# Performance work log

Measured on AMD Instinct MI355X. Metric: run time of the kernel, lower is better.

## Reference

```python
import jax, jax.numpy as jnp
import numpy as np

N_NODES = 50000


def _gcn_conv(x, W, b, src, dst, n):
    # GCNConv (PyG semantics): x' = D^-1/2 (A + I) D^-1/2 (x W) + b
    h = x @ W  # [N, out]
    loop = jnp.arange(n, dtype=src.dtype)
    s = jnp.concatenate([src, loop])  # self-loops appended
    d = jnp.concatenate([dst, loop])
    deg = jax.ops.segment_sum(jnp.ones_like(d, dtype=h.dtype), d, num_segments=n)
    dinv = jnp.where(deg > 0, jax.lax.rsqrt(deg), 0.0)
    norm = dinv[s] * dinv[d]  # [E+N]
    msgs = norm[:, None] * h[s]  # gather: [E+N, out]
    out = jax.ops.segment_sum(msgs, d, num_segments=n)  # scatter-add
    return out + b


def setup_inputs() -> dict:
    key = jax.random.key(0)
    ks = jax.random.split(key, 6)
    n, din, dh, dout, e = N_NODES, 64, 64, 16, 1600000
    x = jax.random.normal(ks[0], (n, din), dtype=jnp.float32)
    edge_index = jax.random.randint(ks[1], (2, e), 0, n, dtype=jnp.int64)
    W1 = jax.random.normal(ks[2], (din, dh), dtype=jnp.float32) / np.sqrt(din)
    b1 = jnp.zeros((dh,), dtype=jnp.float32)
    W2 = jax.random.normal(ks[3], (dh, dout), dtype=jnp.float32) / np.sqrt(dh)
    b2 = jnp.zeros((dout,), dtype=jnp.float32)
    return {"x": x, "edge_index": edge_index, "W1": W1, "b1": b1, "W2": W2, "b2": b2}


def reference(x, edge_index, W1, b1, W2, b2):
    n = x.shape[0]
    src, dst = edge_index[0], edge_index[1]
    h = _gcn_conv(x, W1, b1, src, dst, n)
    h = jax.nn.relu(h)
    h = _gcn_conv(h, W2, b2, src, dst, n)
    return jax.nn.log_softmax(h, axis=1)
```

## Files before the change

### kernel.cpp

```cpp
#include <hip/hip_runtime.h>
#include <hip/hip_bf16.h>
#include <math.h>

#define BSHIFT 6
#define BNODES 64
#define MAXB 1024
#define SORTCAP 4096

__device__ __forceinline__ bool detect_f64(const void* edges, long long nn) {
    const long long* e64 = (const long long*)edges;
    bool ok = true;
#pragma unroll
    for (int i = 0; i < 8; ++i) {
        long long v = e64[i];
        ok = ok && (v >= 0 && v < nn);
    }
    return ok;
}

__device__ __forceinline__ float bf16lo(unsigned int u) {
    return __uint_as_float(u << 16);
}
__device__ __forceinline__ float bf16hi(unsigned int u) {
    return __uint_as_float(u & 0xFFFF0000u);
}
__device__ __forceinline__ float bf16dec(unsigned short u) {
    return __uint_as_float(((unsigned int)u) << 16);
}
__device__ __forceinline__ unsigned short bf16enc(float f) {
    __hip_bfloat16 h = __float2bfloat16(f);
    return *reinterpret_cast<unsigned short*>(&h);
}

__global__ __launch_bounds__(512) void k_hist(const void* edges, long long nn,
                                              long long E, long long epb,
                                              int nbuckets, int nblk, int* partial) {
    __shared__ int cnt[MAXB];
    int t = threadIdx.x;
    int i = blockIdx.x;
    for (int b = t; b < nbuckets; b += 512) cnt[b] = 0;
    __syncthreads();
    bool f64 = detect_f64(edges, nn);
    long long e0 = (long long)i * epb;
    long long e1 = e0 + epb; if (e1 > E) e1 = E;
    for (long long e = e0 + t; e < e1; e += 512) {
        int d = f64 ? (int)((const long long*)edges)[E + e] : ((const int*)edges)[E + e];
        atomicAdd(&cnt[d >> BSHIFT], 1);
    }
    __syncthreads();
    for (int b = t; b < nbuckets; b += 512) partial[b * nblk + i] = cnt[b];
}

__global__ __launch_bounds__(512) void k_scanB(int* partial, int nblk, int* totals) {
    __shared__ int tmp[512];
    int b = blockIdx.x, t = threadIdx.x;
    int v = (t < nblk) ? partial[b * nblk + t] : 0;
    tmp[t] = v;
    __syncthreads();
    for (int off = 1; off < 512; off <<= 1) {
        int a = (t >= off) ? tmp[t - off] : 0;
        __syncthreads();
        tmp[t] += a;
        __syncthreads();
    }
    if (t < nblk) partial[b * nblk + t] = tmp[t] - v;
    if (t == 511) totals[b] = tmp[511];
}

__global__ __launch_bounds__(1024) void k_scan(const int* __restrict__ totals, int nbuckets,
                                               int* base) {
    __shared__ int tmp[MAXB];
    int t = threadIdx.x;
    int v = (t < nbuckets) ? totals[t] : 0;
    tmp[t] = v;
    __syncthreads();
    for (int off = 1; off < MAXB; off <<= 1) {
        int a = (t >= off) ? tmp[t - off] : 0;
        __syncthreads();
        tmp[t] += a;
        __syncthreads();
    }
    if (t < nbuckets) base[t] = tmp[t] - v;
}

__global__ __launch_bounds__(512) void k_place(const void* edges, long long nn,
                                               long long E, long long epb,
                                               int nbuckets, int nblk,
                                               const int* __restrict__ base,
                                               const int* __restrict__ partial,
                                               unsigned int* keys) {
    __shared__ int cur[MAXB];
    int t = threadIdx.x;
    int i = blockIdx.x;
    for (int b = t; b < nbuckets; b += 512) cur[b] = base[b] + partial[b * nblk + i];
    __syncthreads();
    bool f64 = detect_f64(edges, nn);
    long long e0 = (long long)i * epb;
    long long e1 = e0 + epb; if (e1 > E) e1 = E;
    for (long long e = e0 + t; e < e1; e += 512) {
        int s, d;
        if (f64) {
            const long long* ee = (const long long*)edges;
            s = (int)ee[e]; d = (int)ee[E + e];
        } else {
            const int* ee = (const int*)edges;
            s = ee[e]; d = ee[E + e];
        }
        int pos = atomicAdd(&cur[d >> BSHIFT], 1);
        keys[pos] = (unsigned int)s | ((unsigned int)(d & (BNODES - 1)) << 17);
    }
}

__global__ __launch_bounds__(256) void k_sortdeg(unsigned int* keys,
                                                 const int* __restrict__ base,
                                                 const int* __restrict__ totals,
                                                 int* rowstart, int* counts,
                                                 float* dinv, int n,
                                                 unsigned int* scratch) {
    __shared__ unsigned int kbuf[SORTCAP];
    __shared__ int hist[BNODES];
    __shared__ int cur[BNODES];
    int t = threadIdx.x;
    int bk = blockIdx.x;
    int st = base[bk], c = totals[bk];
    if (t < BNODES) hist[t] = 0;
    __syncthreads();
    bool fits = (c <= SORTCAP);
    if (fits) {
        for (int i = t; i < c; i += 256) {
            unsigned int k = keys[st + i];
            kbuf[i] = k;
            atomicAdd(&hist[k >> 17], 1);
        }
    } else {
        for (int i = t; i < c; i += 256) {
            unsigned int k = keys[st + i];
            scratch[st + i] = k;
            atomicAdd(&hist[k >> 17], 1);
        }
    }
    __syncthreads();
    if (t < 64) {
        int v = hist[t];
        int incl = v;
        for (int o = 1; o < 64; o <<= 1) {
            int other = __shfl_up(incl, o, 64);
            if (t >= o) incl += other;
        }
        int ex = incl - v;
        cur[t] = ex;
        int node = bk * BNODES + t;
        if (node < n) {
            rowstart[node] = st + ex;
            counts[node] = v;
            dinv[node] = rsqrtf((float)v + 1.0f);
        }
    }
    __syncthreads();
    if (fits) {
        for (int i = t; i < c; i += 256) {
            unsigned int k = kbuf[i];
            int pos = atomicAdd(&cur[k >> 17], 1);
            keys[st + pos] = k & 0x1FFFFu;
        }
    } else {
        for (int i = t; i < c; i += 256) {
            unsigned int k = scratch[st + i];
            int pos = atomicAdd(&cur[k >> 17], 1);
            keys[st + pos] = k & 0x1FFFFu;
        }
    }
}

__global__ __launch_bounds__(256) void k_gemm1(const float* __restrict__ x,
                                               const float* __restrict__ W,
                                               const float* __restrict__ dinv,
                                               unsigned short* __restrict__ h) {
    __shared__ float Ws[64][64];
    __shared__ float xs[16][64];
    int t = threadIdx.x;
    for (int i = t; i < 64 * 64; i += 256) Ws[i >> 6][i & 63] = W[i];
    long long row0 = (long long)blockIdx.x * 16;
    ((float4*)xs)[t] = ((const float4*)(x + row0 * 64))[t];
    __syncthreads();
    int r = t >> 4, c0 = (t & 15) * 4;
    float4 acc = {0.f, 0.f, 0.f, 0.f};
#pragma unroll
    for (int k = 0; k < 64; ++k) {
        float xv = xs[r][k];
        float4 wv = *((const float4*)&Ws[k][c0]);
        acc.x += xv * wv.x; acc.y += xv * wv.y;
        acc.z += xv * wv.z; acc.w += xv * wv.w;
    }
    float di = dinv[row0 + r];
    ushort4 pk;
    pk.x = bf16enc(di * acc.x);
    pk.y = bf16enc(di * acc.y);
    pk.z = bf16enc(di * acc.z);
    pk.w = bf16enc(di * acc.w);
    *((ushort4*)(h + (row0 + r) * 64 + c0)) = pk;
}

__global__ __launch_bounds__(256) void k_agg64(const int* __restrict__ rowstart,
                                               const int* __restrict__ counts,
                                               const unsigned int* __restrict__ srcs,
                                               const uint2* __restrict__ hb4,
                                               const float* __restrict__ dinv,
                                               const float* __restrict__ b,
                                               const float* __restrict__ W2,
                                               unsigned short* __restrict__ h2b, int n) {
    __shared__ float W2s[64 * 17];
    int t = threadIdx.x;
    for (int i = t; i < 64 * 16; i += 256) W2s[(i >> 4) * 17 + (i & 15)] = W2[i];
    __syncthreads();

    int d = (blockIdx.x * 256 + t) >> 6;
    if (d >= n) return;
    int lane = t & 63;
    unsigned int q = lane >> 4;
    unsigned int fl = lane & 15;
    float a0 = 0.f, a1 = 0.f, a2 = 0.f, a3 = 0.f;
    if (q == 0) {
        uint2 u = hb4[(unsigned int)d * 16u + fl];
        a0 = bf16lo(u.x); a1 = bf16hi(u.x); a2 = bf16lo(u.y); a3 = bf16hi(u.y);
    }
    int start = rowstart[d];
    int cnt = counts[d];
    int k = 0;
    for (; k + 16 <= cnt; k += 16) {
        unsigned int s0 = srcs[start + k + q];
        unsigned int s1 = srcs[start + k + 4 + q];
        unsigned int s2 = srcs[start + k + 8 + q];
        unsigned int s3 = srcs[start + k + 12 + q];
        uint2 u0 = hb4[s0 * 16u + fl];
        uint2 u1 = hb4[s1 * 16u + fl];
        uint2 u2 = hb4[s2 * 16u + fl];
        uint2 u3 = hb4[s3 * 16u + fl];
        a0 += bf16lo(u0.x); a1 += bf16hi(u0.x); a2 += bf16lo(u0.y); a3 += bf16hi(u0.y);
        a0 += bf16lo(u1.x); a1 += bf16hi(u1.x); a2 += bf16lo(u1.y); a3 += bf16hi(u1.y);
        a0 += bf16lo(u2.x); a1 += bf16hi(u2.x); a2 += bf16lo(u2.y); a3 += bf16hi(u2.y);
        a0 += bf16lo(u3.x); a1 += bf16hi(u3.x); a2 += bf16lo(u3.y); a3 += bf16hi(u3.y);
    }
    for (; k + 8 <= cnt; k += 8) {
        unsigned int s0 = srcs[start + k + q];
        unsigned int s1 = srcs[start + k + 4 + q];
        uint2 u0 = hb4[s0 * 16u + fl];
        uint2 u1 = hb4[s1 * 16u + fl];
        a0 += bf16lo(u0.x); a1 += bf16hi(u0.x); a2 += bf16lo(u0.y); a3 += bf16hi(u0.y);
        a0 += bf16lo(u1.x); a1 += bf16hi(u1.x); a2 += bf16lo(u1.y); a3 += bf16hi(u1.y);
    }
    for (; k < cnt; k += 4) {
        int idx = k + (int)q;
        if (idx < cnt) {
            uint2 u0 = hb4[srcs[start + idx] * 16u + fl];
            a0 += bf16lo(u0.x); a1 += bf16hi(u0.x); a2 += bf16lo(u0.y); a3 += bf16hi(u0.y);
        }
    }
    a0 += __shfl_xor(a0, 16); a0 += __shfl_xor(a0, 32);
    a1 += __shfl_xor(a1, 16); a1 += __shfl_xor(a1, 32);
    a2 += __shfl_xor(a2, 16); a2 += __shfl_xor(a2, 32);
    a3 += __shfl_xor(a3, 16); a3 += __shfl_xor(a3, 32);
    float di = dinv[d];
    float4 bb = ((const float4*)b)[fl];
    float o0 = fmaxf(di * a0 + bb.x, 0.f);
    float o1 = fmaxf(di * a1 + bb.y, 0.f);
    float o2 = fmaxf(di * a2 + bb.z, 0.f);
    float o3 = fmaxf(di * a3 + bb.w, 0.f);

    int c = lane & 15;
    float acc = 0.f;
#pragma unroll
    for (int j = 0; j < 16; ++j) {
        int kk = (int)q * 16 + j;
        int srcl = (int)q * 20 + (j >> 2);
        float fv;
        if ((j & 3) == 0)      fv = __shfl(o0, srcl);
        else if ((j & 3) == 1) fv = __shfl(o1, srcl);
        else if ((j & 3) == 2) fv = __shfl(o2, srcl);
        else                   fv = __shfl(o3, srcl);
        acc += fv * W2s[kk * 17 + c];
    }
    acc += __shfl_xor(acc, 16);
    acc += __shfl_xor(acc, 32);
    if (lane < 16) h2b[(unsigned int)d * 16u + c] = bf16enc(di * acc);
}

__global__ __launch_bounds__(256) void k_agg16(const int* __restrict__ rowstart,
                                               const int* __restrict__ counts,
                                               const unsigned int* __restrict__ srcs,
                                               const uint2* __restrict__ hb4,
                                               const float* __restrict__ dinv,
                                               const float* __restrict__ b,
                                               float* __restrict__ out, int n) {
    int g = (blockIdx.x * 256 + threadIdx.x) >> 4;
    if (g >= n) return;
    int lane = threadIdx.x & 15;
    unsigned int eg = lane >> 2;
    unsigned int fp = lane & 3;
    float a0 = 0.f, a1 = 0.f, a2 = 0.f, a3 = 0.f;
    if (eg == 0) {
        uint2 u = hb4[(unsigned int)g * 4u + fp];
        a0 = bf16lo(u.x); a1 = bf16hi(u.x); a2 = bf16lo(u.y); a3 = bf16hi(u.y);
    }
    int start = rowstart[g];
    int cnt = counts[g];
    int k = 0;
    for (; k + 8 <= cnt; k += 8) {
        unsigned int s0 = srcs[start + k + eg];
        unsigned int s1 = srcs[start + k + 4 + eg];
        uint2 u0 = hb4[s0 * 4u + fp];
        uint2 u1 = hb4[s1 * 4u + fp];
        a0 += bf16lo(u0.x); a1 += bf16hi(u0.x); a2 += bf16lo(u0.y); a3 += bf16hi(u0.y);
        a0 += bf16lo(u1.x); a1 += bf16hi(u1.x); a2 += bf16lo(u1.y); a3 += bf16hi(u1.y);
    }
    for (; k < cnt; k += 4) {
        int idx = k + (int)eg;
        if (idx < cnt) {
            uint2 u0 = hb4[srcs[start + idx] * 4u + fp];
            a0 += bf16lo(u0.x); a1 += bf16hi(u0.x); a2 += bf16lo(u0.y); a3 += bf16hi(u0.y);
        }
    }
    a0 += __shfl_xor(a0, 4); a0 += __shfl_xor(a0, 8);
    a1 += __shfl_xor(a1, 4); a1 += __shfl_xor(a1, 8);
    a2 += __shfl_xor(a2, 4); a2 += __shfl_xor(a2, 8);
    a3 += __shfl_xor(a3, 4); a3 += __shfl_xor(a3, 8);
    float di = dinv[g];
    float4 bb = ((const float4*)b)[fp];
    float v0 = di * a0 + bb.x;
    float v1 = di * a1 + bb.y;
    float v2 = di * a2 + bb.z;
    float v3 = di * a3 + bb.w;
    float m = fmaxf(fmaxf(v0, v1), fmaxf(v2, v3));
    m = fmaxf(m, __shfl_xor(m, 1));
    m = fmaxf(m, __shfl_xor(m, 2));
    float ex = __expf(v0 - m) + __expf(v1 - m) + __expf(v2 - m) + __expf(v3 - m);
    ex += __shfl_xor(ex, 1);
    ex += __shfl_xor(ex, 2);
    float lse = __logf(ex) + m;
    if (eg == 0) {
        float4 o4;
        o4.x = v0 - lse; o4.y = v1 - lse; o4.z = v2 - lse; o4.w = v3 - lse;
        ((float4*)(out + (unsigned int)g * 16u))[fp] = o4;
    }
}

extern "C" void kernel_launch(void* const* d_in, const int* in_sizes, int n_in,
                              void* d_out, int out_size, void* d_ws, size_t ws_size,
                              hipStream_t stream) {
    const float* x  = (const float*)d_in[0];
    const void*  ei = d_in[1];
    const float* W1 = (const float*)d_in[2];
    const float* b1 = (const float*)d_in[3];
    const float* W2 = (const float*)d_in[4];
    const float* b2 = (const float*)d_in[5];

    long long dh  = in_sizes[3];
    long long din = in_sizes[2] / dh;
    long long n   = in_sizes[0] / din;
    long long E   = (long long)in_sizes[1] / 2;
    int nbuckets  = (int)((n + BNODES - 1) >> BSHIFT);

    long long epb = 4096;
    while ((E + epb - 1) / epb > 512) epb <<= 1;
    int nblk = (int)((E + epb - 1) / epb);

    char* ws = (char*)d_ws;
    auto alloc = [&](size_t bytes) { void* p = ws; ws += (bytes + 255) & ~255ULL; return p; };
    int*   totals   = (int*)alloc(nbuckets * 4);
    int*   base     = (int*)alloc(nbuckets * 4);
    int*   rowstart = (int*)alloc(n * 4);
    int*   counts   = (int*)alloc(n * 4);
    float* dinv     = (float*)alloc(n * 4);
    int*   partial  = (int*)alloc((size_t)nbuckets * nblk * 4);
    unsigned int* keys = (unsigned int*)alloc(E * 4);
    unsigned short* h1b  = (unsigned short*)alloc(n * 64 * 2);
    unsigned short* h2b  = (unsigned short*)alloc(n * 16 * 2);
    unsigned int* sort_scratch = (unsigned int*)h1b;

    float* out = (float*)d_out;

    k_hist<<<nblk, 512, 0, stream>>>(ei, n, E, epb, nbuckets, nblk, partial);
    k_scanB<<<nbuckets, 512, 0, stream>>>(partial, nblk, totals);
    k_scan<<<1, 1024, 0, stream>>>(totals, nbuckets, base);
    k_place<<<nblk, 512, 0, stream>>>(ei, n, E, epb, nbuckets, nblk, base, partial, keys);
    k_sortdeg<<<nbuckets, 256, 0, stream>>>(keys, base, totals, rowstart, counts,
                                            dinv, (int)n, sort_scratch);

    k_gemm1<<<(int)(n / 16), 256, 0, stream>>>(x, W1, dinv, h1b);
    k_agg64<<<(int)((n * 64 + 255) / 256), 256, 0, stream>>>(
        rowstart, counts, keys, (const uint2*)h1b, dinv, b1, W2, h2b, (int)n);

    k_agg16<<<(int)((n * 16 + 255) / 256), 256, 0, stream>>>(
        rowstart, counts, keys, (const uint2*)h2b, dinv, b2, out, (int)n);
}
```

Baseline: 119.3 us.

## Halve histogram blocks, deepen agg64 unroll, and restructure agg16 per-feature lanes

Edge blocks per histogram/place pass drop from at most 512 to at most 256, with the per-bucket scan shrunk to 256 threads to match. k_agg64 gains a 32-edge unrolled loop to keep more gathers in flight. k_agg16 now gives each lane one feature across all edges instead of splitting edges across lane groups. That removes the cross-lane reduction but issues scalar 2-byte gathers and redundant index loads. Fewer histogram blocks reduce scan work but may lower parallelism in hist/place.

```diff
diff --git a/kernel.cpp b/kernel.cpp
--- a/kernel.cpp
+++ b/kernel.cpp
@@ -51,20 +51,20 @@
     for (int b = t; b < nbuckets; b += 512) partial[b * nblk + i] = cnt[b];
 }
 
-__global__ __launch_bounds__(512) void k_scanB(int* partial, int nblk, int* totals) {
-    __shared__ int tmp[512];
+__global__ __launch_bounds__(256) void k_scanB(int* partial, int nblk, int* totals) {
+    __shared__ int tmp[256];
     int b = blockIdx.x, t = threadIdx.x;
     int v = (t < nblk) ? partial[b * nblk + t] : 0;
     tmp[t] = v;
     __syncthreads();
-    for (int off = 1; off < 512; off <<= 1) {
+    for (int off = 1; off < 256; off <<= 1) {
         int a = (t >= off) ? tmp[t - off] : 0;
         __syncthreads();
         tmp[t] += a;
         __syncthreads();
     }
     if (t < nblk) partial[b * nblk + t] = tmp[t] - v;
-    if (t == 511) totals[b] = tmp[511];
+    if (t == 255) totals[b] = tmp[255];
 }
 
 __global__ __launch_bounds__(1024) void k_scan(const int* __restrict__ totals, int nbuckets,
@@ -227,6 +227,32 @@
     int start = rowstart[d];
     int cnt = counts[d];
     int k = 0;
+    for (; k + 32 <= cnt; k += 32) {
+        unsigned int s0 = srcs[start + k + q];
+        unsigned int s1 = srcs[start + k + 4 + q];
+        unsigned int s2 = srcs[start + k + 8 + q];
+        unsigned int s3 = srcs[start + k + 12 + q];
+        unsigned int s4 = srcs[start + k + 16 + q];
+        unsigned int s5 = srcs[start + k + 20 + q];
+        unsigned int s6 = srcs[start + k + 24 + q];
+        unsigned int s7 = srcs[start + k + 28 + q];
+        uint2 u0 = hb4[s0 * 16u + fl];
+        uint2 u1 = hb4[s1 * 16u + fl];
+        uint2 u2 = hb4[s2 * 16u + fl];
+        uint2 u3 = hb4[s3 * 16u + fl];
+        uint2 u4 = hb4[s4 * 16u + fl];
+        uint2 u5 = hb4[s5 * 16u + fl];
+        uint2 u6 = hb4[s6 * 16u + fl];
+        uint2 u7 = hb4[s7 * 16u + fl];
+        a0 += bf16lo(u0.x); a1 += bf16hi(u0.x); a2 += bf16lo(u0.y); a3 += bf16hi(u0.y);
+        a0 += bf16lo(u1.x); a1 += bf16hi(u1.x); a2 += bf16lo(u1.y); a3 += bf16hi(u1.y);
+        a0 += bf16lo(u2.x); a1 += bf16hi(u2.x); a2 += bf16lo(u2.y); a3 += bf16hi(u2.y);
+        a0 += bf16lo(u3.x); a1 += bf16hi(u3.x); a2 += bf16lo(u3.y); a3 += bf16hi(u3.y);
+        a0 += bf16lo(u4.x); a1 += bf16hi(u4.x); a2 += bf16lo(u4.y); a3 += bf16hi(u4.y);
+        a0 += bf16lo(u5.x); a1 += bf16hi(u5.x); a2 += bf16lo(u5.y); a3 += bf16hi(u5.y);
+        a0 += bf16lo(u6.x); a1 += bf16hi(u6.x); a2 += bf16lo(u6.y); a3 += bf16hi(u6.y);
+        a0 += bf16lo(u7.x); a1 += bf16hi(u7.x); a2 += bf16lo(u7.y); a3 += bf16hi(u7.y);
+    }
     for (; k + 16 <= cnt; k += 16) {
         unsigned int s0 = srcs[start + k + q];
         unsigned int s1 = srcs[start + k + 4 + q];
@@ -288,60 +314,46 @@
 __global__ __launch_bounds__(256) void k_agg16(const int* __restrict__ rowstart,
                                                const int* __restrict__ counts,
                                                const unsigned int* __restrict__ srcs,
-                                               const uint2* __restrict__ hb4,
+                                               const unsigned short* __restrict__ hb,
                                                const float* __restrict__ dinv,
                                                const float* __restrict__ b,
                                                float* __restrict__ out, int n) {
     int g = (blockIdx.x * 256 + threadIdx.x) >> 4;
     if (g >= n) return;
-    int lane = threadIdx.x & 15;
-    unsigned int eg = lane >> 2;
-    unsigned int fp = lane & 3;
-    float a0 = 0.f, a1 = 0.f, a2 = 0.f, a3 = 0.f;
-    if (eg == 0) {
-        uint2 u = hb4[(unsigned int)g * 4u + fp];
-        a0 = bf16lo(u.x); a1 = bf16hi(u.x); a2 = bf16lo(u.y); a3 = bf16hi(u.y);
-    }
+    unsigned int f = threadIdx.x & 15;
+    float acc = bf16dec(hb[(unsigned int)g * 16u + f]);
     int start = rowstart[g];
     int cnt = counts[g];
     int k = 0;
     for (; k + 8 <= cnt; k += 8) {
-        unsigned int s0 = srcs[start + k + eg];
-        unsigned int s1 = srcs[start + k + 4 + eg];
-        uint2 u0 = hb4[s0 * 4u + fp];
-        uint2 u1 = hb4[s1 * 4u + fp];
-        a0 += bf16lo(u0.x); a1 += bf16hi(u0.x); a2 += bf16lo(u0.y); a3 += bf16hi(u0.y);
-        a0 += bf16lo(u1.x); a1 += bf16hi(u1.x); a2 += bf16lo(u1.y); a3 += bf16hi(u1.y);
-    }
-    for (; k < cnt; k += 4) {
-        int idx = k + (int)eg;
-        if (idx < cnt) {
-            uint2 u0 = hb4[srcs[start + idx] * 4u + fp];
-            a0 += bf16lo(u0.x); a1 += bf16hi(u0.x); a2 += bf16lo(u0.y); a3 += bf16hi(u0.y);
-        }
-    }
-    a0 += __shfl_xor(a0, 4); a0 += __shfl_xor(a0, 8);
-    a1 += __shfl_xor(a1, 4); a1 += __shfl_xor(a1, 8);
-    a2 += __shfl_xor(a2, 4); a2 += __shfl_xor(a2, 8);
-    a3 += __shfl_xor(a3, 4); a3 += __shfl_xor(a3, 8);
-    float di = dinv[g];
-    float4 bb = ((const float4*)b)[fp];
-    float v0 = di * a0 + bb.x;
-    float v1 = di * a1 + bb.y;
-    float v2 = di * a2 + bb.z;
-    float v3 = di * a3 + bb.w;
-    float m = fmaxf(fmaxf(v0, v1), fmaxf(v2, v3));
-    m = fmaxf(m, __shfl_xor(m, 1));
-    m = fmaxf(m, __shfl_xor(m, 2));
-    float ex = __expf(v0 - m) + __expf(v1 - m) + __expf(v2 - m) + __expf(v3 - m);
-    ex += __shfl_xor(ex, 1);
-    ex += __shfl_xor(ex, 2);
-    float lse = __logf(ex) + m;
-    if (eg == 0) {
-        float4 o4;
-        o4.x = v0 - lse; o4.y = v1 - lse; o4.z = v2 - lse; o4.w = v3 - lse;
-        ((float4*)(out + (unsigned int)g * 16u))[fp] = o4;
-    }
+        unsigned int s0 = srcs[start + k];
+        unsigned int s1 = srcs[start + k + 1];
+        unsigned int s2 = srcs[start + k + 2];
+        unsigned int s3 = srcs[start + k + 3];
+        unsigned int s4 = srcs[start + k + 4];
+        unsigned int s5 = srcs[start + k + 5];
+        unsigned int s6 = srcs[start + k + 6];
+        unsigned int s7 = srcs[start + k + 7];
+        unsigned short u0 = hb[s0 * 16u + f];
+        unsigned short u1 = hb[s1 * 16u + f];
+        unsigned short u2 = hb[s2 * 16u + f];
+        unsigned short u3 = hb[s3 * 16u + f];
+        unsigned short u4 = hb[s4 * 16u + f];
+        unsigned short u5 = hb[s5 * 16u + f];
+        unsigned short u6 = hb[s6 * 16u + f];
+        unsigned short u7 = hb[s7 * 16u + f];
+        acc += bf16dec(u0); acc += bf16dec(u1); acc += bf16dec(u2); acc += bf16dec(u3);
+        acc += bf16dec(u4); acc += bf16dec(u5); acc += bf16dec(u6); acc += bf16dec(u7);
+    }
+    for (; k < cnt; ++k) acc += bf16dec(hb[srcs[start + k] * 16u + f]);
+    float v = dinv[g] * acc + b[f];
+    float m = v;
+#pragma unroll
+    for (int o = 8; o >= 1; o >>= 1) m = fmaxf(m, __shfl_xor(m, o, 16));
+    float ex = __expf(v - m);
+#pragma unroll
+    for (int o = 8; o >= 1; o >>= 1) ex += __shfl_xor(ex, o, 16);
+    out[(unsigned int)g * 16u + f] = (v - m) - __logf(ex);
 }
 
 extern "C" void kernel_launch(void* const* d_in, const int* in_sizes, int n_in,
@@ -360,8 +372,8 @@
     long long E   = (long long)in_sizes[1] / 2;
     int nbuckets  = (int)((n + BNODES - 1) >> BSHIFT);
 
-    long long epb = 4096;
-    while ((E + epb - 1) / epb > 512) epb <<= 1;
+    long long epb = 8192;
+    while ((E + epb - 1) / epb > 256) epb <<= 1;
     int nblk = (int)((E + epb - 1) / epb);
 
     char* ws = (char*)d_ws;
@@ -380,7 +392,7 @@
     float* out = (float*)d_out;
 
     k_hist<<<nblk, 512, 0, stream>>>(ei, n, E, epb, nbuckets, nblk, partial);
-    k_scanB<<<nbuckets, 512, 0, stream>>>(partial, nblk, totals);
+    k_scanB<<<nbuckets, 256, 0, stream>>>(partial, nblk, totals);
     k_scan<<<1, 1024, 0, stream>>>(totals, nbuckets, base);
     k_place<<<nblk, 512, 0, stream>>>(ei, n, E, epb, nbuckets, nblk, base, partial, keys);
     k_sortdeg<<<nbuckets, 256, 0, stream>>>(keys, base, totals, rowstart, counts,
@@ -391,5 +403,5 @@
         rowstart, counts, keys, (const uint2*)h1b, dinv, b1, W2, h2b, (int)n);
 
     k_agg16<<<(int)((n * 16 + 255) / 256), 256, 0, stream>>>(
-        rowstart, counts, keys, (const uint2*)h2b, dinv, b2, out, (int)n);
-}
+        rowstart, counts, keys, h2b, dinv, b2, out, (int)n);
+}
```

Result: faster. 114.6 us (-4.0%).
